# Kernel tuning notes

Measured on AMD Instinct MI355X. Metric: run time of the kernel, lower is better.

## Reference

```python
import jax, jax.numpy as jnp
import numpy as np

V, E, H, L, B, T = 50000, 512, 512, 32, 64, 512


def _lstm_dir(xg, w_hh, reverse):
    # xg: [B,T,4H] precomputed input-to-gate projections (+ biases)
    b, t, g4 = xg.shape
    h_dim = g4 // 4
    def step(carry, xt):
        h, c = carry
        g = xt + h @ w_hh.T  # [B,4H], PyTorch gate order i,f,g,o
        i, f, gg, o = jnp.split(g, 4, axis=-1)
        c = jax.nn.sigmoid(f) * c + jax.nn.sigmoid(i) * jnp.tanh(gg)
        h = jax.nn.sigmoid(o) * jnp.tanh(c)
        return (h, c), h
    init = (jnp.zeros((b, h_dim), xg.dtype), jnp.zeros((b, h_dim), xg.dtype))
    _, hs = jax.lax.scan(step, init, jnp.swapaxes(xg, 0, 1), reverse=reverse)
    return jnp.swapaxes(hs, 0, 1)  # [B,T,H]


def _bilstm(x, w_ih0, w_ih1, w_hh, b_ih, b_hh):
    w_ihs = (w_ih0, w_ih1)
    for l in range(2):
        outs = []
        for d in range(2):  # 0=forward, 1=backward
            xg = jnp.einsum('bti,gi->btg', x, w_ihs[l][d]) + b_ih[l, d] + b_hh[l, d]
            outs.append(_lstm_dir(xg, w_hh[l, d], reverse=(d == 1)))
        x = jnp.concatenate(outs, axis=-1)  # [B,T,2H]
    return x


def _crf_nll(emissions, tags, start, end, trans):
    # pytorch-crf: returns sum log-likelihood; module returns its negation.
    emit = jnp.take_along_axis(emissions, tags[..., None], axis=-1)[..., 0]  # [B,T]
    num = (start[tags[:, 0]] + emit.sum(1)
           + trans[tags[:, :-1], tags[:, 1:]].sum(1) + end[tags[:, -1]])
    alpha0 = start + emissions[:, 0]  # [B,L]
    def step(alpha, e_t):
        s = alpha[:, :, None] + trans[None] + e_t[:, None, :]  # [B,L,L]
        return jax.nn.logsumexp(s, axis=1), None
    alpha, _ = jax.lax.scan(step, alpha0, jnp.swapaxes(emissions[:, 1:], 0, 1))
    denom = jax.nn.logsumexp(alpha + end, axis=-1)  # [B]
    return -(num - denom).sum()


def setup_inputs() -> dict:
    key = jax.random.key(0)
    ks = jax.random.split(key, 13)
    s = 0.05
    emb = jax.random.normal(ks[0], (V, E), jnp.float32) * s
    emb = emb.at[0].set(0.0)  # padding_idx=0
    return {
        'datas': jax.random.randint(ks[1], (B, T), 0, V, jnp.int32),
        'labels': jax.random.randint(ks[2], (B, T), 0, L, jnp.int32),
        'emb': emb,
        'w_ih0': jax.random.normal(ks[3], (2, 4 * H, E), jnp.float32) * s,
        'w_ih1': jax.random.normal(ks[4], (2, 4 * H, 2 * H), jnp.float32) * s,
        'w_hh': jax.random.normal(ks[5], (2, 2, 4 * H, H), jnp.float32) * s,
        'b_ih': jax.random.normal(ks[6], (2, 2, 4 * H), jnp.float32) * s,
        'b_hh': jax.random.normal(ks[7], (2, 2, 4 * H), jnp.float32) * s,
        'w_out': jax.random.normal(ks[8], (2 * H, L), jnp.float32) * s,
        'b_out': jax.random.normal(ks[9], (L,), jnp.float32) * s,
        'crf_start': jax.random.normal(ks[10], (L,), jnp.float32) * s,
        'crf_end': jax.random.normal(ks[11], (L,), jnp.float32) * s,
        'crf_trans': jax.random.normal(ks[12], (L, L), jnp.float32) * s,
    }


def reference(datas, labels, emb, w_ih0, w_ih1, w_hh, b_ih, b_hh, w_out, b_out,
              crf_start, crf_end, crf_trans):
    x = emb[datas]  # [B,T,E]
    h = _bilstm(x, w_ih0, w_ih1, w_hh, b_ih, b_hh)  # [B,T,2H]; dropout=0 (eval)
    emissions = h @ w_out + b_out  # [B,T,L]
    return _crf_nll(emissions, labels, crf_start, crf_end, crf_trans)
```

## Files before the change

kernel.cpp:

```cpp
#include <hip/hip_runtime.h>

typedef unsigned short ushort_t;
typedef unsigned long long u64_t;
typedef __attribute__((ext_vector_type(8))) short short8;
typedef __attribute__((ext_vector_type(4))) float floatx4;


__device__ __forceinline__ float bf2f(ushort_t u) {
  unsigned x = ((unsigned)u) << 16;
  return __builtin_bit_cast(float, x);
}
__device__ __forceinline__ ushort_t f2bf(float f) {
  unsigned x = __builtin_bit_cast(unsigned, f);
  x += 0x7FFFu + ((x >> 16) & 1u);
  return (ushort_t)(x >> 16);
}
__device__ __forceinline__ float sigf(float x) { return 1.0f / (1.0f + __expf(-x)); }
__device__ __forceinline__ float tanhf_(float x) { return 1.0f - 2.0f / (__expf(2.0f * x) + 1.0f); }

static const size_t OFF_A    = 0;
static const size_t OFF_OUT0 = 67108864;
static const size_t OFF_XG   = 134217728;
static const size_t OFF_WIH0 = 167772160;
static const size_t OFF_WIH1 = 171966464;
static const size_t OFF_BIAS = 180355072;
static const size_t OFF_WOUT = 180387840;
static const size_t OFF_HC   = 180453376;
static const size_t OFF_CST  = 181501952;
static const size_t OFF_BAR  = 182026240;
static const size_t OFF_NUM  = 182034432;
static const size_t OFF_PERB = 182034688;
static const size_t OFF_END  = 182034944;

__global__ void prep_kernel(const float* __restrict__ w_ih0, const float* __restrict__ w_ih1,
                            const float* __restrict__ b_ih, const float* __restrict__ b_hh,
                            const float* __restrict__ w_out,
                            ushort_t* __restrict__ wih0_bf, ushort_t* __restrict__ wih1_bf,
                            float* __restrict__ bias, ushort_t* __restrict__ wout_bf) {
  int idx = blockIdx.x * 256 + threadIdx.x;
  int stride = gridDim.x * 256;
  for (int i = idx; i < 2097152; i += stride) wih0_bf[i] = f2bf(w_ih0[i]);
  for (int i = idx; i < 4194304; i += stride) wih1_bf[i] = f2bf(w_ih1[i]);
  for (int i = idx; i < 8192; i += stride) bias[i] = b_ih[i] + b_hh[i];
  for (int i = idx; i < 32768; i += stride) {
    int j = i & 7, Ls = (i >> 3) & 63, kb = (i >> 9) & 31, nt = i >> 14;
    int n = nt * 16 + (Ls & 15);
    int k = kb * 32 + ((Ls >> 4) & 3) * 8 + j;
    wout_bf[i] = f2bf(w_out[k * 32 + n]);
  }
}

__global__ void embed_kernel(const int* __restrict__ datas, const float* __restrict__ emb,
                             ushort_t* __restrict__ x_bf) {
  int idx = blockIdx.x * 256 + threadIdx.x;
  int row = idx >> 6, sub = idx & 63;
  int tok = datas[row];
  const float4* ep = (const float4*)(emb + (size_t)tok * 512 + sub * 8);
  float4 f0 = ep[0], f1 = ep[1];
  short8 v;
  v[0] = (short)f2bf(f0.x); v[1] = (short)f2bf(f0.y);
  v[2] = (short)f2bf(f0.z); v[3] = (short)f2bf(f0.w);
  v[4] = (short)f2bf(f1.x); v[5] = (short)f2bf(f1.y);
  v[6] = (short)f2bf(f1.z); v[7] = (short)f2bf(f1.w);
  *(short8*)(x_bf + (size_t)row * 512 + sub * 8) = v;
}

__global__ __launch_bounds__(256) void gemm_chunk(const ushort_t* __restrict__ A, int K,
                                                  const ushort_t* __restrict__ W,
                                                  const float* __restrict__ biasL,
                                                  ushort_t* __restrict__ xg0c,
                                                  ushort_t* __restrict__ xg1c,
                                                  int t00, int t01) {
  __shared__ alignas(16) ushort_t alds[512 * 8];
  __shared__ alignas(16) ushort_t blds[512 * 8];
  int gid = blockIdx.x;
  int dir = gid >> 9, r = gid & 511;
  int mt = r & 31, ntt = r >> 5;
  int t0 = dir ? t01 : t00;
  const ushort_t* Bm = W + (size_t)dir * 2048 * K;
  const float* bptr = biasL + dir * 2048;
  ushort_t* xg = dir ? xg1c : xg0c;
  int bm0 = mt * 128, bn0 = ntt * 128;
  int tid = threadIdx.x, L = tid & 63, w = tid >> 6;
  int wm = w & 1, wn = w >> 1;
  floatx4 acc[4][4] = {};
  for (int k0 = 0; k0 < K; k0 += 32) {
    __syncthreads();
    #pragma unroll
    for (int rep = 0; rep < 2; rep++) {
      int slot = rep * 256 + tid;
      int t8 = slot >> 6, Ls = slot & 63;
      int col = k0 + (Ls >> 4) * 8;
      int mp = bm0 + t8 * 16 + (Ls & 15);
      int Arow = (mp >> 6) * 512 + t0 + (mp & 63);
      *(short8*)&alds[slot * 8] = *(const short8*)&A[(size_t)Arow * K + col];
      int rowb = bn0 + t8 * 16 + (Ls & 15);
      *(short8*)&blds[slot * 8] = *(const short8*)&Bm[(size_t)rowb * K + col];
    }
    __syncthreads();
    short8 af[4];
    #pragma unroll
    for (int a = 0; a < 4; a++) af[a] = *(const short8*)&alds[((wm * 4 + a) * 64 + L) * 8];
    #pragma unroll
    for (int bq = 0; bq < 4; bq++) {
      short8 bfr = *(const short8*)&blds[((wn * 4 + bq) * 64 + L) * 8];
      #pragma unroll
      for (int a = 0; a < 4; a++)
        acc[a][bq] = __builtin_amdgcn_mfma_f32_16x16x32_bf16(af[a], bfr, acc[a][bq], 0, 0, 0);
    }
  }
  int lm = L >> 4, ln = L & 15;
  #pragma unroll
  for (int bq = 0; bq < 4; bq++) {
    int n = bn0 + (wn * 4 + bq) * 16 + ln;
    float bv = bptr[n];
    #pragma unroll
    for (int a = 0; a < 4; a++) {
      #pragma unroll
      for (int rr = 0; rr < 4; rr++) {
        int m = bm0 + (wm * 4 + a) * 16 + lm * 4 + rr;
        int b = m >> 6, ts = m & 63;
        xg[((size_t)(ts * 64 + b)) * 2048 + n] = f2bf(acc[a][bq][rr] + bv);
      }
    }
  }
}

__global__ __launch_bounds__(256) void lstm_chunk(const ushort_t* __restrict__ xg0c,
                                                  const ushort_t* __restrict__ xg1c,
                                                  const float* __restrict__ whh_f,
                                                  ushort_t* __restrict__ hcL,
                                                  float* __restrict__ cstL,
                                                  ushort_t* __restrict__ outL,
                                                  int* __restrict__ barF, int c) {
  __shared__ alignas(16) ushort_t wlds[32768];
  int bid = blockIdx.x, d = bid >> 5, g = bid & 31, j0 = g * 16;
  int tid = threadIdx.x, L = tid & 63, w = tid >> 6;
  const float* wptr = whh_f + (size_t)d * 2048 * 512;
  #pragma unroll
  for (int it = 0; it < 16; it++) {
    int slot = it * 256 + tid;
    int q = slot >> 10, kb = (slot >> 6) & 15, Ls = slot & 63;
    int gcol = q * 512 + j0 + (Ls & 15);
    int k = kb * 32 + (Ls >> 4) * 8;
    const float* src = wptr + (size_t)gcol * 512 + k;
    float4 f0 = *(const float4*)src;
    float4 f1 = *(const float4*)(src + 4);
    short8 v;
    v[0] = (short)f2bf(f0.x); v[1] = (short)f2bf(f0.y);
    v[2] = (short)f2bf(f0.z); v[3] = (short)f2bf(f0.w);
    v[4] = (short)f2bf(f1.x); v[5] = (short)f2bf(f1.y);
    v[6] = (short)f2bf(f1.z); v[7] = (short)f2bf(f1.w);
    *(short8*)&wlds[slot * 8] = v;
  }
  __syncthreads();
  const ushort_t* xgd = d ? xg1c : xg0c;
  ushort_t* hcd = hcL + (size_t)d * 2 * 32768;
  int* flg = barF + d * 512;
  int* myflag = flg + g * 16;
  int q8 = L >> 4, jj = L & 15;
  int mbase = w * 16 + q8 * 4;
  int wslot = ((w * 16 + (g >> 1)) * 64 + q8 * 4 + 16 * ((g & 1) * 2 + (jj >> 3))) * 8 + (jj & 7);
  int rbase = (w * 16 * 64 + L) * 8;
  float cv[4];
  #pragma unroll
  for (int rr = 0; rr < 4; rr++) cv[rr] = cstL[(size_t)d * 32768 + (mbase + rr) * 512 + j0 + jj];

  auto ldxg = [&](int sl2, ushort_t dst[4][4]) {
    int ts2 = d ? (63 - sl2) : sl2;
    #pragma unroll
    for (int rr = 0; rr < 4; rr++) {
      const ushort_t* xrow = xgd + ((size_t)(ts2 * 64 + mbase + rr)) * 2048 + j0 + jj;
      #pragma unroll
      for (int q = 0; q < 4; q++) dst[q][rr] = xrow[q * 512];
    }
  };

  ushort_t xgu[4][4];
  ldxg(0, xgu);

  for (int sl = 0; sl < 64; sl++) {
    int s = c * 64 + sl;
    int t = d ? (511 - s) : s;
    const u64_t* h64 = (const u64_t*)(hcd + (size_t)(s & 1) * 32768);
    unsigned* h32w = (unsigned*)(hcd + (size_t)((s + 1) & 1) * 32768);
    int b64 = rbase >> 2;
    u64_t hv[32];
    #pragma unroll
    for (int kb = 0; kb < 16; kb++) {
      hv[2 * kb]     = __hip_atomic_load(h64 + b64 + kb * 128,     __ATOMIC_RELAXED, __HIP_MEMORY_SCOPE_SYSTEM);
      hv[2 * kb + 1] = __hip_atomic_load(h64 + b64 + kb * 128 + 1, __ATOMIC_RELAXED, __HIP_MEMORY_SCOPE_SYSTEM);
    }
    floatx4 acc[4] = {};
    #pragma unroll
    for (int kb = 0; kb < 16; kb++) {
      union { u64_t u[2]; short8 v; } pk;
      pk.u[0] = hv[2 * kb];
      pk.u[1] = hv[2 * kb + 1];
      short8 a = pk.v;
      #pragma unroll
      for (int q = 0; q < 4; q++) {
        short8 bfr = *(const short8*)&wlds[((q * 16 + kb) * 64 + L) * 8];
        acc[q] = __builtin_amdgcn_mfma_f32_16x16x32_bf16(a, bfr, acc[q], 0, 0, 0);
      }
    }
    ushort_t hbv[4];
    #pragma unroll
    for (int rr = 0; rr < 4; rr++) {
      float ii = acc[0][rr] + bf2f(xgu[0][rr]);
      float ff = acc[1][rr] + bf2f(xgu[1][rr]);
      float gg = acc[2][rr] + bf2f(xgu[2][rr]);
      float oo = acc[3][rr] + bf2f(xgu[3][rr]);
      float cc = sigf(ff) * cv[rr] + sigf(ii) * tanhf_(gg);
      cv[rr] = cc;
      hbv[rr] = f2bf(sigf(oo) * tanhf_(cc));
    }
    bool evn = (jj & 1) == 0;
    #pragma unroll
    for (int rr = 0; rr < 4; rr++) {
      unsigned mine = (unsigned)hbv[rr];
      unsigned nb = (unsigned)__shfl_xor((int)mine, 1, 64);
      if (evn) {
        unsigned packed = mine | (nb << 16);
        __hip_atomic_store(h32w + ((wslot + rr * 8) >> 1), packed,
                           __ATOMIC_RELAXED, __HIP_MEMORY_SCOPE_SYSTEM);
        int m = mbase + rr;
        *(unsigned*)&outL[((size_t)m * 512 + t) * 1024 + (d << 9) + j0 + jj] = packed;
      }
    }
    if (sl != 63) {
      ldxg(sl + 1, xgu);
      __builtin_amdgcn_s_waitcnt(0);
      __syncthreads();
      if (tid == 0)
        __hip_atomic_store(myflag, s + 1, __ATOMIC_RELAXED, __HIP_MEMORY_SCOPE_SYSTEM);
      if (tid < 64) {
        int target = s + 1, guard = 0;
        while (guard < (1 << 17)) {
          int f = __hip_atomic_load(flg + (tid & 31) * 16, __ATOMIC_RELAXED, __HIP_MEMORY_SCOPE_SYSTEM);
          if (__ballot(f >= target) == ~0ULL) break;
          guard++;
        }
      }
      __syncthreads();
    }
  }
  #pragma unroll
  for (int rr = 0; rr < 4; rr++) cstL[(size_t)d * 32768 + (mbase + rr) * 512 + j0 + jj] = cv[rr];
}

__global__ __launch_bounds__(256) void emis_kernel(const ushort_t* __restrict__ out1,
                                                   const ushort_t* __restrict__ wout_bf,
                                                   const float* __restrict__ b_out,
                                                   float* __restrict__ emis) {
  int tid = threadIdx.x, L = tid & 63, w = tid >> 6;
  int bm0 = blockIdx.x * 128;
  int q8 = L >> 4, ln = L & 15;
  floatx4 acc[2][2] = {};
  #pragma unroll 4
  for (int kb = 0; kb < 32; kb++) {
    short8 a0 = *(const short8*)&out1[(size_t)(bm0 + (w * 2 + 0) * 16 + ln) * 1024 + kb * 32 + q8 * 8];
    short8 a1 = *(const short8*)&out1[(size_t)(bm0 + (w * 2 + 1) * 16 + ln) * 1024 + kb * 32 + q8 * 8];
    #pragma unroll
    for (int nt = 0; nt < 2; nt++) {
      short8 bfr = *(const short8*)&wout_bf[((size_t)(nt * 32 + kb) * 64 + L) * 8];
      acc[0][nt] = __builtin_amdgcn_mfma_f32_16x16x32_bf16(a0, bfr, acc[0][nt], 0, 0, 0);
      acc[1][nt] = __builtin_amdgcn_mfma_f32_16x16x32_bf16(a1, bfr, acc[1][nt], 0, 0, 0);
    }
  }
  #pragma unroll
  for (int mt = 0; mt < 2; mt++) {
    #pragma unroll
    for (int nt = 0; nt < 2; nt++) {
      int n = nt * 16 + ln;
      float bv = b_out[n];
      #pragma unroll
      for (int rr = 0; rr < 4; rr++) {
        int m = bm0 + (w * 2 + mt) * 16 + q8 * 4 + rr;
        emis[(size_t)m * 32 + n] = acc[mt][nt][rr] + bv;
      }
    }
  }
}

__global__ void num_kernel(const int* __restrict__ labels, const float* __restrict__ emis,
                           const float* __restrict__ trans, const float* __restrict__ cstart,
                           const float* __restrict__ cend, float* __restrict__ num) {
  int b = blockIdx.x, tid = threadIdx.x;
  float s = 0.f;
  for (int t = tid; t < 512; t += 64) {
    int tag = labels[b * 512 + t];
    s += emis[(size_t)(b * 512 + t) * 32 + tag];
    if (t < 511) s += trans[tag * 32 + labels[b * 512 + t + 1]];
  }
  #pragma unroll
  for (int off = 32; off > 0; off >>= 1) s += __shfl_xor(s, off, 64);
  if (tid == 0) num[b] = s + cstart[labels[b * 512]] + cend[labels[b * 512 + 511]];
}

__global__ __launch_bounds__(64) void fwd_kernel(const float* __restrict__ emis,
                                                 const float* __restrict__ trans,
                                                 const float* __restrict__ cstart,
                                                 const float* __restrict__ cend,
                                                 const float* __restrict__ num,
                                                 float* __restrict__ perb) {
  int b = blockIdx.x, tid = threadIdx.x, j = tid & 31;
  float trj[32];
  #pragma unroll
  for (int i = 0; i < 32; i++) trj[i] = trans[i * 32 + j];
  float alpha = cstart[j] + emis[(size_t)(b * 512) * 32 + j];
  for (int t = 1; t < 512; t++) {
    float e = emis[(size_t)(b * 512 + t) * 32 + j];
    float m = -1e30f;
    float v[32];
    #pragma unroll
    for (int i = 0; i < 32; i++) {
      v[i] = __shfl(alpha, i, 32) + trj[i];
      m = fmaxf(m, v[i]);
    }
    float s = 0.f;
    #pragma unroll
    for (int i = 0; i < 32; i++) s += __expf(v[i] - m);
    alpha = __logf(s) + m + e;
  }
  float z = alpha + cend[j];
  float m2 = z;
  #pragma unroll
  for (int off = 16; off > 0; off >>= 1) m2 = fmaxf(m2, __shfl_xor(m2, off, 32));
  float s2 = __expf(z - m2);
  #pragma unroll
  for (int off = 16; off > 0; off >>= 1) s2 += __shfl_xor(s2, off, 32);
  if (tid == 0) perb[b] = num[b] - (__logf(s2) + m2);
}

__global__ void final_kernel(const float* __restrict__ perb, float* __restrict__ out) {
  int tid = threadIdx.x;
  float s = perb[tid];
  #pragma unroll
  for (int off = 32; off > 0; off >>= 1) s += __shfl_xor(s, off, 64);
  if (tid == 0) out[0] = -s;
}

extern "C" void kernel_launch(void* const* d_in, const int* in_sizes, int n_in,
                              void* d_out, int out_size, void* d_ws, size_t ws_size,
                              hipStream_t stream) {
  (void)in_sizes; (void)n_in; (void)out_size; (void)ws_size;
  const int* datas = (const int*)d_in[0];
  const int* labels = (const int*)d_in[1];
  const float* emb = (const float*)d_in[2];
  const float* w_ih0 = (const float*)d_in[3];
  const float* w_ih1 = (const float*)d_in[4];
  const float* w_hh = (const float*)d_in[5];
  const float* b_ih = (const float*)d_in[6];
  const float* b_hh = (const float*)d_in[7];
  const float* w_out = (const float*)d_in[8];
  const float* b_out = (const float*)d_in[9];
  const float* cstart = (const float*)d_in[10];
  const float* cend = (const float*)d_in[11];
  const float* ctrans = (const float*)d_in[12];

  char* ws = (char*)d_ws;
  ushort_t* x_bf = (ushort_t*)(ws + OFF_A);
  ushort_t* out1 = (ushort_t*)(ws + OFF_A);
  ushort_t* out0 = (ushort_t*)(ws + OFF_OUT0);
  ushort_t* xg0c = (ushort_t*)(ws + OFF_XG);
  ushort_t* xg1c = (ushort_t*)(ws + OFF_XG + 16777216);
  float* emis = (float*)(ws + OFF_XG);
  ushort_t* wih0_bf = (ushort_t*)(ws + OFF_WIH0);
  ushort_t* wih1_bf = (ushort_t*)(ws + OFF_WIH1);
  float* bias = (float*)(ws + OFF_BIAS);
  ushort_t* wout_bf = (ushort_t*)(ws + OFF_WOUT);
  ushort_t* hc0 = (ushort_t*)(ws + OFF_HC);
  ushort_t* hc1 = hc0 + 131072;
  float* cst0 = (float*)(ws + OFF_CST);
  float* cst1 = cst0 + 65536;
  int* bar = (int*)(ws + OFF_BAR);
  float* numb = (float*)(ws + OFF_NUM);
  float* perb = (float*)(ws + OFF_PERB);

  hipMemsetAsync(ws + OFF_HC, 0, OFF_END - OFF_HC, stream);

  prep_kernel<<<2048, 256, 0, stream>>>(w_ih0, w_ih1, b_ih, b_hh, w_out,
                                        wih0_bf, wih1_bf, bias, wout_bf);
  embed_kernel<<<8192, 256, 0, stream>>>(datas, emb, x_bf);

  for (int c = 0; c < 8; c++) {
    gemm_chunk<<<1024, 256, 0, stream>>>(x_bf, 512, wih0_bf, bias, xg0c, xg1c,
                                         c * 64, (7 - c) * 64);
    lstm_chunk<<<64, 256, 0, stream>>>(xg0c, xg1c, w_hh, hc0, cst0, out0, bar, c);
  }
  for (int c = 0; c < 8; c++) {
    gemm_chunk<<<1024, 256, 0, stream>>>(out0, 1024, wih1_bf, bias + 4096, xg0c, xg1c,
                                         c * 64, (7 - c) * 64);
    lstm_chunk<<<64, 256, 0, stream>>>(xg0c, xg1c, w_hh + 2097152, hc1, cst1, out1,
                                       bar + 1024, c);
  }

  emis_kernel<<<256, 256, 0, stream>>>(out1, wout_bf, b_out, emis);
  num_kernel<<<64, 64, 0, stream>>>(labels, emis, ctrans, cstart, cend, numb);
  fwd_kernel<<<64, 64, 0, stream>>>(emis, ctrans, cstart, cend, numb, perb);
  final_kernel<<<1, 64, 0, stream>>>(perb, (float*)d_out);
}
```

Measured before the change: 5.835 ms.

## Replace LSTM grid barrier with step-tagged hidden state words; CRF forward via exp-space matvec

The persistent LSTM kernel now stores each bf16 hidden value in a 32-bit word together with a 16-bit step tag. Consumers spin on exactly the words they need instead of using a per-step flag barrier with two __syncthreads. This removes the global all-block barrier and lets blocks proceed as soon as their inputs are ready, at the cost of doubling hidden-state traffic and register pressure (64 u64 loads per lane). The CRF forward recursion is also rewritten as a max-shifted exponent-space matrix-vector product, cutting exp calls per step from 32 to 1 but with some numerical range risk.

```diff
diff --git a/kernel.cpp b/kernel.cpp
--- a/kernel.cpp
+++ b/kernel.cpp
@@ -27,10 +27,9 @@
 static const size_t OFF_WOUT = 180387840;
 static const size_t OFF_HC   = 180453376;
 static const size_t OFF_CST  = 181501952;
-static const size_t OFF_BAR  = 182026240;
-static const size_t OFF_NUM  = 182034432;
-static const size_t OFF_PERB = 182034688;
-static const size_t OFF_END  = 182034944;
+static const size_t OFF_NUM  = 182026240;
+static const size_t OFF_PERB = 182026496;
+static const size_t OFF_END  = 182026752;
 
 __global__ void prep_kernel(const float* __restrict__ w_ih0, const float* __restrict__ w_ih1,
                             const float* __restrict__ b_ih, const float* __restrict__ b_hh,
@@ -126,13 +125,13 @@
   }
 }
 
-__global__ __launch_bounds__(256) void lstm_chunk(const ushort_t* __restrict__ xg0c,
-                                                  const ushort_t* __restrict__ xg1c,
-                                                  const float* __restrict__ whh_f,
-                                                  ushort_t* __restrict__ hcL,
-                                                  float* __restrict__ cstL,
-                                                  ushort_t* __restrict__ outL,
-                                                  int* __restrict__ barF, int c) {
+__global__ __launch_bounds__(256, 1) void lstm_chunk(const ushort_t* __restrict__ xg0c,
+                                                     const ushort_t* __restrict__ xg1c,
+                                                     const float* __restrict__ whh_f,
+                                                     unsigned* __restrict__ hcL,
+                                                     float* __restrict__ cstL,
+                                                     ushort_t* __restrict__ outL,
+                                                     int c) {
   __shared__ alignas(16) ushort_t wlds[32768];
   int bid = blockIdx.x, d = bid >> 5, g = bid & 31, j0 = g * 16;
   int tid = threadIdx.x, L = tid & 63, w = tid >> 6;
@@ -140,8 +139,8 @@
   #pragma unroll
   for (int it = 0; it < 16; it++) {
     int slot = it * 256 + tid;
-    int q = slot >> 10, kb = (slot >> 6) & 15, Ls = slot & 63;
-    int gcol = q * 512 + j0 + (Ls & 15);
+    int qg = slot >> 10, kb = (slot >> 6) & 15, Ls = slot & 63;
+    int gcol = qg * 512 + j0 + (Ls & 15);
     int k = kb * 32 + (Ls >> 4) * 8;
     const float* src = wptr + (size_t)gcol * 512 + k;
     float4 f0 = *(const float4*)src;
@@ -155,53 +154,67 @@
   }
   __syncthreads();
   const ushort_t* xgd = d ? xg1c : xg0c;
-  ushort_t* hcd = hcL + (size_t)d * 2 * 32768;
-  int* flg = barF + d * 512;
-  int* myflag = flg + g * 16;
+  unsigned* hcd = hcL + (size_t)d * 2 * 32768;
   int q8 = L >> 4, jj = L & 15;
   int mbase = w * 16 + q8 * 4;
-  int wslot = ((w * 16 + (g >> 1)) * 64 + q8 * 4 + 16 * ((g & 1) * 2 + (jj >> 3))) * 8 + (jj & 7);
-  int rbase = (w * 16 * 64 + L) * 8;
+  int rb = w * 16 * 256 + q8 * 64 + jj * 4;
+  int wb = (w * 16 + (g >> 1)) * 512 + ((g & 1) * 2 + (jj >> 3)) * 128 + q8 * 32 + (jj & 7);
+  const u64_t TMASK = 0x0000FFFF0000FFFFull;
   float cv[4];
   #pragma unroll
   for (int rr = 0; rr < 4; rr++) cv[rr] = cstL[(size_t)d * 32768 + (mbase + rr) * 512 + j0 + jj];
-
-  auto ldxg = [&](int sl2, ushort_t dst[4][4]) {
-    int ts2 = d ? (63 - sl2) : sl2;
-    #pragma unroll
-    for (int rr = 0; rr < 4; rr++) {
-      const ushort_t* xrow = xgd + ((size_t)(ts2 * 64 + mbase + rr)) * 2048 + j0 + jj;
-      #pragma unroll
-      for (int q = 0; q < 4; q++) dst[q][rr] = xrow[q * 512];
-    }
-  };
-
-  ushort_t xgu[4][4];
-  ldxg(0, xgu);
 
   for (int sl = 0; sl < 64; sl++) {
     int s = c * 64 + sl;
     int t = d ? (511 - s) : s;
+    int ts = d ? (63 - sl) : sl;
     const u64_t* h64 = (const u64_t*)(hcd + (size_t)(s & 1) * 32768);
-    unsigned* h32w = (unsigned*)(hcd + (size_t)((s + 1) & 1) * 32768);
-    int b64 = rbase >> 2;
-    u64_t hv[32];
+    unsigned* hw = hcd + (size_t)((s + 1) & 1) * 32768;
+    u64_t tag2 = ((u64_t)(unsigned)s) | ((u64_t)(unsigned)s << 32);
+    u64_t hv[64];
     #pragma unroll
     for (int kb = 0; kb < 16; kb++) {
-      hv[2 * kb]     = __hip_atomic_load(h64 + b64 + kb * 128,     __ATOMIC_RELAXED, __HIP_MEMORY_SCOPE_SYSTEM);
-      hv[2 * kb + 1] = __hip_atomic_load(h64 + b64 + kb * 128 + 1, __ATOMIC_RELAXED, __HIP_MEMORY_SCOPE_SYSTEM);
+      #pragma unroll
+      for (int qq = 0; qq < 4; qq++)
+        hv[kb * 4 + qq] = __hip_atomic_load(h64 + rb + kb * 256 + qq,
+                                            __ATOMIC_RELAXED, __HIP_MEMORY_SCOPE_SYSTEM);
+    }
+    ushort_t xgu[4][4];
+    #pragma unroll
+    for (int rr = 0; rr < 4; rr++) {
+      const ushort_t* xrow = xgd + ((size_t)(ts * 64 + mbase + rr)) * 2048 + j0 + jj;
+      #pragma unroll
+      for (int qg = 0; qg < 4; qg++) xgu[qg][rr] = xrow[qg * 512];
+    }
+    u64_t pend = 0;
+    #pragma unroll
+    for (int i = 0; i < 64; i++)
+      if (((hv[i] ^ tag2) & TMASK) != 0) pend |= (1ull << i);
+    int guard = 0;
+    while (pend != 0 && guard < (1 << 20)) {
+      #pragma unroll
+      for (int i = 0; i < 64; i++) {
+        if ((pend >> i) & 1) {
+          u64_t v = __hip_atomic_load(h64 + rb + (i >> 2) * 256 + (i & 3),
+                                      __ATOMIC_RELAXED, __HIP_MEMORY_SCOPE_SYSTEM);
+          if (((v ^ tag2) & TMASK) == 0) { hv[i] = v; pend &= ~(1ull << i); }
+        }
+      }
+      guard++;
     }
     floatx4 acc[4] = {};
     #pragma unroll
     for (int kb = 0; kb < 16; kb++) {
-      union { u64_t u[2]; short8 v; } pk;
-      pk.u[0] = hv[2 * kb];
-      pk.u[1] = hv[2 * kb + 1];
-      short8 a = pk.v;
-      #pragma unroll
-      for (int q = 0; q < 4; q++) {
-        short8 bfr = *(const short8*)&wlds[((q * 16 + kb) * 64 + L) * 8];
-        acc[q] = __builtin_amdgcn_mfma_f32_16x16x32_bf16(a, bfr, acc[q], 0, 0, 0);
+      union { unsigned u[4]; short8 v8; } af;
+      #pragma unroll
+      for (int qq = 0; qq < 4; qq++) {
+        u64_t h = hv[kb * 4 + qq];
+        af.u[qq] = (unsigned)((h >> 16) & 0xffffu) | (unsigned)((h >> 32) & 0xffff0000u);
+      }
+      #pragma unroll
+      for (int qg = 0; qg < 4; qg++) {
+        short8 bfr = *(const short8*)&wlds[((qg * 16 + kb) * 64 + L) * 8];
+        acc[qg] = __builtin_amdgcn_mfma_f32_16x16x32_bf16(af.v8, bfr, acc[qg], 0, 0, 0);
       }
     }
     ushort_t hbv[4];
@@ -215,6 +228,11 @@
       cv[rr] = cc;
       hbv[rr] = f2bf(sigf(oo) * tanhf_(cc));
     }
+    unsigned tagw = (unsigned)(s + 1) & 0xffffu;
+    #pragma unroll
+    for (int rr = 0; rr < 4; rr++)
+      __hip_atomic_store(hw + wb + rr * 8, ((unsigned)hbv[rr] << 16) | tagw,
+                         __ATOMIC_RELAXED, __HIP_MEMORY_SCOPE_SYSTEM);
     bool evn = (jj & 1) == 0;
     #pragma unroll
     for (int rr = 0; rr < 4; rr++) {
@@ -222,27 +240,9 @@
       unsigned nb = (unsigned)__shfl_xor((int)mine, 1, 64);
       if (evn) {
         unsigned packed = mine | (nb << 16);
-        __hip_atomic_store(h32w + ((wslot + rr * 8) >> 1), packed,
-                           __ATOMIC_RELAXED, __HIP_MEMORY_SCOPE_SYSTEM);
         int m = mbase + rr;
         *(unsigned*)&outL[((size_t)m * 512 + t) * 1024 + (d << 9) + j0 + jj] = packed;
       }
-    }
-    if (sl != 63) {
-      ldxg(sl + 1, xgu);
-      __builtin_amdgcn_s_waitcnt(0);
-      __syncthreads();
-      if (tid == 0)
-        __hip_atomic_store(myflag, s + 1, __ATOMIC_RELAXED, __HIP_MEMORY_SCOPE_SYSTEM);
-      if (tid < 64) {
-        int target = s + 1, guard = 0;
-        while (guard < (1 << 17)) {
-          int f = __hip_atomic_load(flg + (tid & 31) * 16, __ATOMIC_RELAXED, __HIP_MEMORY_SCOPE_SYSTEM);
-          if (__ballot(f >= target) == ~0ULL) break;
-          guard++;
-        }
-      }
-      __syncthreads();
     }
   }
   #pragma unroll
@@ -305,23 +305,25 @@
                                                  const float* __restrict__ num,
                                                  float* __restrict__ perb) {
   int b = blockIdx.x, tid = threadIdx.x, j = tid & 31;
-  float trj[32];
-  #pragma unroll
-  for (int i = 0; i < 32; i++) trj[i] = trans[i * 32 + j];
+  float Pj[32];
+  #pragma unroll
+  for (int i = 0; i < 32; i++) Pj[i] = __expf(trans[i * 32 + j]);
   float alpha = cstart[j] + emis[(size_t)(b * 512) * 32 + j];
   for (int t = 1; t < 512; t++) {
     float e = emis[(size_t)(b * 512 + t) * 32 + j];
-    float m = -1e30f;
-    float v[32];
-    #pragma unroll
-    for (int i = 0; i < 32; i++) {
-      v[i] = __shfl(alpha, i, 32) + trj[i];
-      m = fmaxf(m, v[i]);
-    }
-    float s = 0.f;
-    #pragma unroll
-    for (int i = 0; i < 32; i++) s += __expf(v[i] - m);
-    alpha = __logf(s) + m + e;
+    float M = alpha;
+    #pragma unroll
+    for (int off = 16; off > 0; off >>= 1) M = fmaxf(M, __shfl_xor(M, off, 32));
+    float A = __expf(alpha - M);
+    float s0 = 0.f, s1 = 0.f, s2 = 0.f, s3 = 0.f;
+    #pragma unroll
+    for (int i = 0; i < 32; i += 4) {
+      s0 += __shfl(A, i, 32) * Pj[i];
+      s1 += __shfl(A, i + 1, 32) * Pj[i + 1];
+      s2 += __shfl(A, i + 2, 32) * Pj[i + 2];
+      s3 += __shfl(A, i + 3, 32) * Pj[i + 3];
+    }
+    alpha = __logf((s0 + s1) + (s2 + s3)) + M + e;
   }
   float z = alpha + cend[j];
   float m2 = z;
@@ -370,11 +372,10 @@
   ushort_t* wih1_bf = (ushort_t*)(ws + OFF_WIH1);
   float* bias = (float*)(ws + OFF_BIAS);
   ushort_t* wout_bf = (ushort_t*)(ws + OFF_WOUT);
-  ushort_t* hc0 = (ushort_t*)(ws + OFF_HC);
-  ushort_t* hc1 = hc0 + 131072;
+  unsigned* hc0 = (unsigned*)(ws + OFF_HC);
+  unsigned* hc1 = hc0 + 131072;
   float* cst0 = (float*)(ws + OFF_CST);
   float* cst1 = cst0 + 65536;
-  int* bar = (int*)(ws + OFF_BAR);
   float* numb = (float*)(ws + OFF_NUM);
   float* perb = (float*)(ws + OFF_PERB);
 
@@ -387,13 +388,12 @@
   for (int c = 0; c < 8; c++) {
     gemm_chunk<<<1024, 256, 0, stream>>>(x_bf, 512, wih0_bf, bias, xg0c, xg1c,
                                          c * 64, (7 - c) * 64);
-    lstm_chunk<<<64, 256, 0, stream>>>(xg0c, xg1c, w_hh, hc0, cst0, out0, bar, c);
+    lstm_chunk<<<64, 256, 0, stream>>>(xg0c, xg1c, w_hh, hc0, cst0, out0, c);
   }
   for (int c = 0; c < 8; c++) {
     gemm_chunk<<<1024, 256, 0, stream>>>(out0, 1024, wih1_bf, bias + 4096, xg0c, xg1c,
                                          c * 64, (7 - c) * 64);
-    lstm_chunk<<<64, 256, 0, stream>>>(xg0c, xg1c, w_hh + 2097152, hc1, cst1, out1,
-                                       bar + 1024, c);
+    lstm_chunk<<<64, 256, 0, stream>>>(xg0c, xg1c, w_hh + 2097152, hc1, cst1, out1, c);
   }
 
   emis_kernel<<<256, 256, 0, stream>>>(out1, wout_bf, b_out, emis);
```

Measured after the change: 16.41 ms. 2.81x slower.
